# Optimization experiments

Measured on AMD Instinct MI355X. Metric: run time of the kernel, lower is better.

Reference implementation:

```python
import jax, jax.numpy as jnp
import numpy as np

EPS = 1e-5
NH, KD, D = 16, 16, 64  # num_heads, key_dim, per-head value dim (attn_ratio*key_dim)


def _bn(x, g, b):
    # train-mode BatchNorm1d over [B, C, N]: stats over (B, N), biased variance
    m = jnp.mean(x, axis=(0, 2), keepdims=True)
    v = jnp.var(x, axis=(0, 2), keepdims=True)
    return (x - m) * jax.lax.rsqrt(v + EPS) * g[None, :, None] + b[None, :, None]


def _relu6(x):
    return jnp.clip(x, 0.0, 6.0)


def setup_inputs() -> dict:
    key = jax.random.key(0)
    ks = jax.random.split(key, 8)
    B, C, H, W = 8, 256, 32, 32
    dim, dh, hid = 256, NH * D, 1024

    def w(k, shape):
        return jax.random.normal(k, shape, dtype=jnp.float32) * 0.02

    return {
        "x": jax.random.normal(ks[0], (B, C, H, W), dtype=jnp.float32),
        "g1": jnp.ones((dim,), jnp.float32), "b1": jnp.zeros((dim,), jnp.float32),
        "wq": w(ks[1], (NH * KD, dim)), "bq": jnp.zeros((NH * KD,), jnp.float32),
        "wk": w(ks[2], (NH * KD, dim)), "bk": jnp.zeros((NH * KD,), jnp.float32),
        "wv": w(ks[3], (dh, dim)), "bv": jnp.zeros((dh,), jnp.float32),
        "wp": w(ks[4], (dim, dh)), "bp": jnp.zeros((dim,), jnp.float32),
        "g2": jnp.ones((dim,), jnp.float32), "b2": jnp.zeros((dim,), jnp.float32),
        "w1": w(ks[5], (hid, dim)), "bb1": jnp.zeros((hid,), jnp.float32),
        "w2": w(ks[6], (dim, hid)), "bb2": jnp.zeros((dim,), jnp.float32),
    }


def reference(x, g1, b1, wq, bq, wk, bk, wv, bv, wp, bp, g2, b2, w1, bb1, w2, bb2):
    B, C, H, W = x.shape
    N = H * W
    xf = x.reshape(B, C, N)

    # --- attention branch (dropout is identity in eval/reference) ---
    y = _bn(xf, g1, b1)
    q = (jnp.einsum('bcn,oc->bon', y, wq) + bq[None, :, None]).reshape(B, NH, KD, N).transpose(0, 1, 3, 2)  # [B,h,N,kd]
    k = jnp.einsum('bcn,oc->bon', y, wk) + bk[None, :, None]
    k = k.reshape(B, NH, KD, N)                                                                           # [B,h,kd,N]
    v = (jnp.einsum('bcn,oc->bon', y, wv) + bv[None, :, None]).reshape(B, NH, D, N).transpose(0, 1, 3, 2)  # [B,h,N,d]
    # torch code divides by scale = key_dim**-0.5, i.e. multiplies by sqrt(key_dim)
    attn = jax.nn.softmax(jnp.einsum('bhnk,bhkm->bhnm', q, k) / (KD ** -0.5), axis=-1)
    o = jnp.einsum('bhnm,bhmd->bhnd', attn, v).transpose(0, 1, 3, 2).reshape(B, NH * D, N)                 # [B,dh,N]
    o = jnp.einsum('bdn,od->bon', o, wp) + bp[None, :, None]                                               # [B,C,N]
    xf = xf + o

    # --- MLP branch: Linear(dim->hid) + ReLU6 + Conv1d(hid->dim, k=1) ---
    y2 = _bn(xf, g2, b2)
    h = _relu6(jnp.einsum('bcn,hc->bhn', y2, w1) + bb1[None, :, None])
    m = jnp.einsum('bhn,oh->bon', h, w2) + bb2[None, :, None]
    xf = xf + m

    return xf.reshape(B, C, H, W)
```

## Files before the change

kernel.cpp:

```cpp
#include <hip/hip_runtime.h>
#include <hip/hip_bf16.h>
#include <cstdint>


typedef __attribute__((ext_vector_type(8))) short short8;
typedef __attribute__((ext_vector_type(4))) float floatx4;

#define QK_SC 5.770780163555851f

__device__ __forceinline__ float b2f(unsigned short u) {
  union { unsigned int i; float f; } x; x.i = ((unsigned int)u) << 16; return x.f;
}
__device__ __forceinline__ unsigned short f2b(float f) {
  union { float f; unsigned int i; } x; x.f = f;
  unsigned int r = x.i + 0x7FFFu + ((x.i >> 16) & 1u);
  return (unsigned short)(r >> 16);
}
__device__ __forceinline__ unsigned int f2b2(float a, float b) {
  __hip_bfloat162 h = __float22bfloat162_rn(make_float2(a, b));
  union { __hip_bfloat162 v; unsigned int u; } x; x.v = h; return x.u;
}
__device__ __forceinline__ void gload16(const unsigned short* g, unsigned short* l) {
  __builtin_amdgcn_global_load_lds(
      (const __attribute__((address_space(1))) unsigned int*)g,
      (__attribute__((address_space(3))) unsigned int*)l, 16, 0, 0);
}

__global__ __launch_bounds__(256) void prep(
    const float* __restrict__ s0, const float* __restrict__ s1,
    const float* __restrict__ s2, const float* __restrict__ s3,
    const float* __restrict__ s4, const float* __restrict__ s5,
    unsigned short* __restrict__ dst,
    const float* __restrict__ x, float* __restrict__ acc,
    const float* __restrict__ bq, const float* __restrict__ bk,
    const float* __restrict__ bv, float* __restrict__ biasqkv) {
  int blk = blockIdx.x, t = threadIdx.x;
  if (blk < 1152) {
    int i = blk * 256 + t;
    if (i >= 294912) return;
    const float* s; int li; size_t dbase;
    if (i < 16384)       { s = s0; li = i;          dbase = 0; }
    else if (i < 32768)  { s = s1; li = i - 16384;  dbase = 65536; }
    else if (i < 98304)  { s = s2; li = i - 32768;  dbase = 131072; }
    else if (i < 163840) { s = s3; li = i - 98304;  dbase = 393216; }
    else if (i < 229376) { s = s4; li = i - 163840; dbase = 655360; }
    else                 { s = s5; li = i - 229376; dbase = 917504; }
    float4 v = ((const float4*)s)[li];
    uint2 o; o.x = f2b2(v.x, v.y); o.y = f2b2(v.z, v.w);
    ((uint2*)(dst + dbase))[li] = o;
  } else if (blk < 3200) {
    int blk2 = blk - 1152;
    int b = blk2 >> 8, c = blk2 & 255;
    const float* p = x + (((size_t)(b * 256 + c)) << 10);
    float4 v = ((const float4*)p)[t];
    float s = (v.x + v.y) + (v.z + v.w);
    float s2 = (v.x * v.x + v.y * v.y) + (v.z * v.z + v.w * v.w);
    #pragma unroll
    for (int o = 32; o > 0; o >>= 1) { s += __shfl_down(s, o, 64); s2 += __shfl_down(s2, o, 64); }
    __shared__ float rs[4], rs2[4];
    int w = t >> 6;
    if ((t & 63) == 0) { rs[w] = s; rs2[w] = s2; }
    __syncthreads();
    if (t == 0) {
      atomicAdd(acc + c, (rs[0] + rs[1]) + (rs[2] + rs[3]));
      atomicAdd(acc + 256 + c, (rs2[0] + rs2[1]) + (rs2[2] + rs2[3]));
    }
  } else {
    int i = (blk - 3200) * 256 + t;
    float v = (i < 256) ? bq[i] : (i < 512) ? bk[i - 256] : bv[i - 512];
    biasqkv[i] = v;
  }
}

__global__ __launch_bounds__(256) void bn_apply_t(
    const float* __restrict__ x, const float* __restrict__ acc,
    const float* __restrict__ g, const float* __restrict__ bb,
    unsigned short* __restrict__ yt) {
  int nt = blockIdx.x, ct = blockIdx.y, b = blockIdx.z;
  int t = threadIdx.x;
  __shared__ unsigned short T[64][72];
  {
    int r = t >> 2, g4 = (t & 3) * 16;
    int c = ct * 64 + r;
    float m = acc[c] * (1.0f / 8192.0f);
    float var = acc[256 + c] * (1.0f / 8192.0f) - m * m;
    float scl = g[c] * rsqrtf(var + 1e-5f);
    float shf = bb[c] - m * scl;
    const float* p = x + (((size_t)(b * 256 + c)) << 10) + nt * 64 + g4;
    float4 u0 = *(const float4*)(p);
    float4 u1 = *(const float4*)(p + 4);
    float4 u2 = *(const float4*)(p + 8);
    float4 u3 = *(const float4*)(p + 12);
    uint4 o0, o1;
    o0.x = f2b2(fmaf(u0.x, scl, shf), fmaf(u0.y, scl, shf));
    o0.y = f2b2(fmaf(u0.z, scl, shf), fmaf(u0.w, scl, shf));
    o0.z = f2b2(fmaf(u1.x, scl, shf), fmaf(u1.y, scl, shf));
    o0.w = f2b2(fmaf(u1.z, scl, shf), fmaf(u1.w, scl, shf));
    o1.x = f2b2(fmaf(u2.x, scl, shf), fmaf(u2.y, scl, shf));
    o1.y = f2b2(fmaf(u2.z, scl, shf), fmaf(u2.w, scl, shf));
    o1.z = f2b2(fmaf(u3.x, scl, shf), fmaf(u3.y, scl, shf));
    o1.w = f2b2(fmaf(u3.z, scl, shf), fmaf(u3.w, scl, shf));
    *(uint4*)&T[r][g4] = o0;
    *(uint4*)&T[r][g4 + 8] = o1;
  }
  __syncthreads();
  {
    int nr = t >> 2, cg = (t & 3) * 16;
    unsigned int ob[8];
    #pragma unroll
    for (int j = 0; j < 8; ++j) {
      unsigned int lo = T[cg + 2 * j][nr];
      unsigned int hi = T[cg + 2 * j + 1][nr];
      ob[j] = lo | (hi << 16);
    }
    unsigned short* orow = yt + ((size_t)(b * 1024 + nt * 64 + nr)) * 256 + ct * 64 + cg;
    *(uint4*)&orow[0] = make_uint4(ob[0], ob[1], ob[2], ob[3]);
    *(uint4*)&orow[8] = make_uint4(ob[4], ob[5], ob[6], ob[7]);
  }
}

template <int MODE>
__global__ __launch_bounds__(256, 4) void gemm3(
    const unsigned short* __restrict__ W, const unsigned short* __restrict__ Bn,
    const float* __restrict__ bias, const float* __restrict__ resf,
    const unsigned short* __restrict__ resb, void* __restrict__ outv,
    float* __restrict__ stats, const float* __restrict__ bnin,
    const float* __restrict__ g, const float* __restrict__ bb, int M, int K) {
  int bid = blockIdx.x;
  int b = bid & 7;
  int rest = bid >> 3;
  int n0 = (rest & 15) * 64, m0 = (rest >> 4) * 64;
  int t = threadIdx.x, lane = t & 63, w = t >> 6;
  int ml = lane & 15, quad = lane >> 4;

  __shared__ unsigned short Wt[64][64];
  __shared__ unsigned short Yt[64][64];
  __shared__ float Scl[256], Shf[256];

  if (MODE == 6) {
    float m = bnin[t] * (1.0f / 8192.0f);
    float var = bnin[256 + t] * (1.0f / 8192.0f) - m * m;
    float scl = g[t] * rsqrtf(var + 1e-5f);
    Scl[t] = scl;
    Shf[t] = bb[t] - m * scl;
    __syncthreads();
  }

  const unsigned short* Bp = Bn + (size_t)b * 1024 * K;
  int sr = t >> 2, scg = (t & 3) * 16;
  const unsigned short* brow = Bp + (size_t)(n0 + sr) * K + scg;

  int lrow = lane >> 3;
  int cgs  = (lane & 7) ^ lrow;

  char* Wb = (char*)&Wt[0][0];
  char* Yb = (char*)&Yt[0][0];
  const int swa = (ml & 7) << 4;

  floatx4 acc[4];
  #pragma unroll
  for (int i = 0; i < 4; ++i) acc[i] = (floatx4){0.f, 0.f, 0.f, 0.f};

  for (int k0 = 0; k0 < K; k0 += 64) {
    #pragma unroll
    for (int j = 0; j < 2; ++j) {
      int row = w * 16 + j * 8 + lrow;
      gload16(W + (size_t)(m0 + row) * K + k0 + cgs * 8, &Wt[w * 16 + j * 8][0]);
    }
    if (MODE == 6) {
      uint4 r0 = *(const uint4*)(brow + k0);
      uint4 r1 = *(const uint4*)(brow + k0 + 8);
      int cb = k0 + scg;
      float4 s0 = *(const float4*)&Scl[cb],     h0 = *(const float4*)&Shf[cb];
      float4 s1 = *(const float4*)&Scl[cb + 4], h1 = *(const float4*)&Shf[cb + 4];
      float4 s2 = *(const float4*)&Scl[cb + 8], h2 = *(const float4*)&Shf[cb + 8];
      float4 s3 = *(const float4*)&Scl[cb + 12], h3 = *(const float4*)&Shf[cb + 12];
      uint4 o0, o1;
      o0.x = f2b2(fmaf(b2f(r0.x & 0xffff), s0.x, h0.x), fmaf(b2f(r0.x >> 16), s0.y, h0.y));
      o0.y = f2b2(fmaf(b2f(r0.y & 0xffff), s0.z, h0.z), fmaf(b2f(r0.y >> 16), s0.w, h0.w));
      o0.z = f2b2(fmaf(b2f(r0.z & 0xffff), s1.x, h1.x), fmaf(b2f(r0.z >> 16), s1.y, h1.y));
      o0.w = f2b2(fmaf(b2f(r0.w & 0xffff), s1.z, h1.z), fmaf(b2f(r0.w >> 16), s1.w, h1.w));
      o1.x = f2b2(fmaf(b2f(r1.x & 0xffff), s2.x, h2.x), fmaf(b2f(r1.x >> 16), s2.y, h2.y));
      o1.y = f2b2(fmaf(b2f(r1.y & 0xffff), s2.z, h2.z), fmaf(b2f(r1.y >> 16), s2.w, h2.w));
      o1.z = f2b2(fmaf(b2f(r1.z & 0xffff), s3.x, h3.x), fmaf(b2f(r1.z >> 16), s3.y, h3.y));
      o1.w = f2b2(fmaf(b2f(r1.w & 0xffff), s3.z, h3.z), fmaf(b2f(r1.w >> 16), s3.w, h3.w));
      int sg0 = (t & 3) * 2, sg1 = sg0 + 1;
      *(uint4*)(Yb + sr * 128 + ((sg0 ^ (sr & 7)) << 4)) = o0;
      *(uint4*)(Yb + sr * 128 + ((sg1 ^ (sr & 7)) << 4)) = o1;
    } else {
      #pragma unroll
      for (int j = 0; j < 2; ++j) {
        int row = w * 16 + j * 8 + lrow;
        gload16(Bp + (size_t)(n0 + row) * K + k0 + cgs * 8, &Yt[w * 16 + j * 8][0]);
      }
    }
    __syncthreads();
    int arow = w * 16 + ml;
    short8 a0 = *(const short8*)(Wb + arow * 128 + ((quad << 4) ^ swa));
    short8 a1 = *(const short8*)(Wb + arow * 128 + (((quad + 4) << 4) ^ swa));
    #pragma unroll
    for (int nt2 = 0; nt2 < 4; ++nt2) {
      int brw = nt2 * 16 + ml;
      short8 b0 = *(const short8*)(Yb + brw * 128 + ((quad << 4) ^ swa));
      short8 b1 = *(const short8*)(Yb + brw * 128 + (((quad + 4) << 4) ^ swa));
      acc[nt2] = __builtin_amdgcn_mfma_f32_16x16x32_bf16(a0, b0, acc[nt2], 0, 0, 0);
      acc[nt2] = __builtin_amdgcn_mfma_f32_16x16x32_bf16(a1, b1, acc[nt2], 0, 0, 0);
    }
    __syncthreads();
  }

  int row_base = m0 + w * 16 + quad * 4;

  if (MODE == 4) {
    int hh = row_base >> 4;
    float b0 = bias[row_base + 0], b1 = bias[row_base + 1];
    float b2 = bias[row_base + 2], b3 = bias[row_base + 3];
    if (hh < 32) {
      unsigned short* qkout = (unsigned short*)outv + ((hh < 16) ? 0 : 2097152);
      float os = (hh < 16) ? QK_SC : 1.0f;
      int head = hh & 15, kd0 = row_base & 15;
      #pragma unroll
      for (int c = 0; c < 4; ++c) {
        int col = n0 + c * 16 + ml;
        uint2 pw;
        pw.x = f2b2((acc[c][0] + b0) * os, (acc[c][1] + b1) * os);
        pw.y = f2b2((acc[c][2] + b2) * os, (acc[c][3] + b3) * os);
        *(uint2*)&qkout[(((size_t)b * 16 + head) * 1024 + col) * 16 + kd0] = pw;
      }
    } else {
      unsigned short* vout = (unsigned short*)outv + 4194304;
      int d0 = row_base - 512;
      #pragma unroll
      for (int c = 0; c < 4; ++c) {
        int col = n0 + c * 16 + ml;
        vout[((size_t)b * 1024 + d0 + 0) * 1024 + col] = f2b(acc[c][0] + b0);
        vout[((size_t)b * 1024 + d0 + 1) * 1024 + col] = f2b(acc[c][1] + b1);
        vout[((size_t)b * 1024 + d0 + 2) * 1024 + col] = f2b(acc[c][2] + b2);
        vout[((size_t)b * 1024 + d0 + 3) * 1024 + col] = f2b(acc[c][3] + b3);
      }
    }
  } else if (MODE == 5) {
    unsigned short* outp = (unsigned short*)outv;
    float vsum[4] = {0.f, 0.f, 0.f, 0.f}, vsq[4] = {0.f, 0.f, 0.f, 0.f};
    #pragma unroll
    for (int c = 0; c < 4; ++c) {
      int col = n0 + c * 16 + ml;
      float v0 = acc[c][0] + bias[row_base + 0] + resf[((size_t)b * 256 + row_base + 0) * 1024 + col];
      float v1 = acc[c][1] + bias[row_base + 1] + resf[((size_t)b * 256 + row_base + 1) * 1024 + col];
      float v2 = acc[c][2] + bias[row_base + 2] + resf[((size_t)b * 256 + row_base + 2) * 1024 + col];
      float v3 = acc[c][3] + bias[row_base + 3] + resf[((size_t)b * 256 + row_base + 3) * 1024 + col];
      vsum[0] += v0; vsq[0] += v0 * v0;
      vsum[1] += v1; vsq[1] += v1 * v1;
      vsum[2] += v2; vsq[2] += v2 * v2;
      vsum[3] += v3; vsq[3] += v3 * v3;
      uint2 pw; pw.x = f2b2(v0, v1); pw.y = f2b2(v2, v3);
      *(uint2*)&outp[((size_t)b * 1024 + col) * 256 + row_base] = pw;
    }
    #pragma unroll
    for (int r = 0; r < 4; ++r) {
      float s = vsum[r], q = vsq[r];
      #pragma unroll
      for (int o = 1; o < 16; o <<= 1) { s += __shfl_xor(s, o, 64); q += __shfl_xor(q, o, 64); }
      if (ml == 0) {
        atomicAdd(stats + row_base + r, s);
        atomicAdd(stats + 256 + row_base + r, q);
      }
    }
  } else if (MODE == 6) {
    unsigned short* outp = (unsigned short*)outv;
    #pragma unroll
    for (int c = 0; c < 4; ++c) {
      int col = n0 + c * 16 + ml;
      float v0 = fminf(fmaxf(acc[c][0] + bias[row_base + 0], 0.f), 6.f);
      float v1 = fminf(fmaxf(acc[c][1] + bias[row_base + 1], 0.f), 6.f);
      float v2 = fminf(fmaxf(acc[c][2] + bias[row_base + 2], 0.f), 6.f);
      float v3 = fminf(fmaxf(acc[c][3] + bias[row_base + 3], 0.f), 6.f);
      uint2 pw; pw.x = f2b2(v0, v1); pw.y = f2b2(v2, v3);
      *(uint2*)&outp[((size_t)b * 1024 + col) * 1024 + row_base] = pw;
    }
  } else {
    float* outp = (float*)outv;
    #pragma unroll
    for (int c = 0; c < 4; ++c) {
      int col = n0 + c * 16 + ml;
      uint2 rv = *(const uint2*)(resb + ((size_t)b * 1024 + col) * 256 + row_base);
      float r0 = b2f((unsigned short)(rv.x & 0xffff));
      float r1 = b2f((unsigned short)(rv.x >> 16));
      float r2 = b2f((unsigned short)(rv.y & 0xffff));
      float r3 = b2f((unsigned short)(rv.y >> 16));
      outp[((size_t)b * 256 + row_base + 0) * 1024 + col] = acc[c][0] + bias[row_base + 0] + r0;
      outp[((size_t)b * 256 + row_base + 1) * 1024 + col] = acc[c][1] + bias[row_base + 1] + r1;
      outp[((size_t)b * 256 + row_base + 2) * 1024 + col] = acc[c][2] + bias[row_base + 2] + r2;
      outp[((size_t)b * 256 + row_base + 3) * 1024 + col] = acc[c][3] + bias[row_base + 3] + r3;
    }
  }
}

__global__ __launch_bounds__(256, 4) void attn_kernel(
    const unsigned short* __restrict__ qt, const unsigned short* __restrict__ kt,
    const unsigned short* __restrict__ vt, unsigned short* __restrict__ ot) {
  int bx0 = blockIdx.x;
  int bx = (bx0 & 7) * 128 + (bx0 >> 3);
  int nt = bx & 7, h = (bx >> 3) & 15, b = bx >> 7;
  int tid = threadIdx.x, lane = tid & 63, w = tid >> 6;
  int ml = lane & 15, quad = lane >> 4;

  __shared__ unsigned int Pscr[4][2][2][16][18];
  __shared__ float Ssum[4][2][16];

  const int n0 = nt * 128 + w * 32;
  const size_t qk_row = ((size_t)b * 16 + h) * 1024;

  short8 qf[2];
  #pragma unroll
  for (int rg = 0; rg < 2; ++rg) {
    short8 z = {0, 0, 0, 0, 0, 0, 0, 0};
    if (quad < 2)
      z = *(const short8*)(qt + (qk_row + n0 + rg * 16 + ml) * 16 + quad * 8);
    qf[rg] = z;
  }

  const floatx4 zf = {0.f, 0.f, 0.f, 0.f};
  floatx4 oacc[2][4];
  #pragma unroll
  for (int rg = 0; rg < 2; ++rg)
    #pragma unroll
    for (int dt = 0; dt < 4; ++dt) oacc[rg][dt] = zf;
  float psum0 = 0.f, psum1 = 0.f;

  const unsigned short* kp = kt + qk_row * 16;
  const unsigned short* vp = vt + ((size_t)b * 1024 + h * 64) * 1024;

  #pragma unroll 2
  for (int mc = 0; mc < 1024; mc += 32) {
    int buf = (mc >> 5) & 1;
    short8 kf[2];
    #pragma unroll
    for (int tt = 0; tt < 2; ++tt) {
      short8 z = {0, 0, 0, 0, 0, 0, 0, 0};
      if (quad < 2)
        z = *(const short8*)(kp + (size_t)(mc + tt * 16 + ml) * 16 + quad * 8);
      kf[tt] = z;
    }
    short8 vf[4];
    #pragma unroll
    for (int dt = 0; dt < 4; ++dt)
      vf[dt] = *(const short8*)(vp + (size_t)(dt * 16 + ml) * 1024 + mc + quad * 8);

    #pragma unroll
    for (int rg = 0; rg < 2; ++rg) {
      #pragma unroll
      for (int tt = 0; tt < 2; ++tt) {
        floatx4 s = __builtin_amdgcn_mfma_f32_16x16x32_bf16(kf[tt], qf[rg], zf, 0, 0, 0);
        float p0 = __builtin_amdgcn_exp2f(s[0]);
        float p1 = __builtin_amdgcn_exp2f(s[1]);
        float p2 = __builtin_amdgcn_exp2f(s[2]);
        float p3 = __builtin_amdgcn_exp2f(s[3]);
        if (rg == 0) psum0 += (p0 + p1) + (p2 + p3);
        else         psum1 += (p0 + p1) + (p2 + p3);
        uint2 pw; pw.x = f2b2(p0, p1); pw.y = f2b2(p2, p3);
        *(uint2*)&Pscr[w][buf][rg][ml][tt * 8 + quad * 2] = pw;
      }
    }
    #pragma unroll
    for (int rg = 0; rg < 2; ++rg) {
      uint2 a0 = *(const uint2*)&Pscr[w][buf][rg][ml][quad * 4];
      uint2 a1 = *(const uint2*)&Pscr[w][buf][rg][ml][quad * 4 + 2];
      union { uint4 u; short8 s; } cv;
      cv.u = make_uint4(a0.x, a0.y, a1.x, a1.y);
      short8 af = cv.s;
      #pragma unroll
      for (int dt = 0; dt < 4; ++dt)
        oacc[rg][dt] = __builtin_amdgcn_mfma_f32_16x16x32_bf16(af, vf[dt], oacc[rg][dt], 0, 0, 0);
    }
  }

  {
    float s0 = psum0;
    s0 += __shfl_xor(s0, 16, 64);
    s0 += __shfl_xor(s0, 32, 64);
    float s1 = psum1;
    s1 += __shfl_xor(s1, 16, 64);
    s1 += __shfl_xor(s1, 32, 64);
    if (lane < 16) { Ssum[w][0][ml] = s0; Ssum[w][1][ml] = s1; }
  }
  #pragma unroll
  for (int rg = 0; rg < 2; ++rg) {
    float4 sv = *(const float4*)&Ssum[w][rg][quad * 4];
    float inv0 = 1.0f / sv.x, inv1 = 1.0f / sv.y;
    float inv2 = 1.0f / sv.z, inv3 = 1.0f / sv.w;
    int nbase = n0 + rg * 16 + quad * 4;
    #pragma unroll
    for (int dt = 0; dt < 4; ++dt) {
      int dg = h * 64 + dt * 16 + ml;
      size_t obase = (((size_t)b << 10) + nbase) * 1024 + dg;
      ot[obase + 0 * 1024] = f2b(oacc[rg][dt][0] * inv0);
      ot[obase + 1 * 1024] = f2b(oacc[rg][dt][1] * inv1);
      ot[obase + 2 * 1024] = f2b(oacc[rg][dt][2] * inv2);
      ot[obase + 3 * 1024] = f2b(oacc[rg][dt][3] * inv3);
    }
  }
}

extern "C" void kernel_launch(void* const* d_in, const int* in_sizes, int n_in,
                              void* d_out, int out_size, void* d_ws, size_t ws_size,
                              hipStream_t stream) {
  const float* x   = (const float*)d_in[0];
  const float* g1  = (const float*)d_in[1];
  const float* b1  = (const float*)d_in[2];
  const float* wq  = (const float*)d_in[3];
  const float* bq  = (const float*)d_in[4];
  const float* wk  = (const float*)d_in[5];
  const float* bk  = (const float*)d_in[6];
  const float* wv  = (const float*)d_in[7];
  const float* bv  = (const float*)d_in[8];
  const float* wp  = (const float*)d_in[9];
  const float* bp  = (const float*)d_in[10];
  const float* g2  = (const float*)d_in[11];
  const float* b2  = (const float*)d_in[12];
  const float* w1  = (const float*)d_in[13];
  const float* bb1 = (const float*)d_in[14];
  const float* w2  = (const float*)d_in[15];
  const float* bb2 = (const float*)d_in[16];

  char* ws = (char*)d_ws;
  float* bnacc   = (float*)ws;
  float* biasqkv = (float*)(ws + 4096);
  unsigned short* y_t  = (unsigned short*)(ws + 16384);
  unsigned short* qt   = y_t + (size_t)2 * 1024 * 1024;
  unsigned short* kt   = qt  + (size_t)2 * 1024 * 1024;
  unsigned short* vt   = kt  + (size_t)2 * 1024 * 1024;
  unsigned short* ot   = vt  + (size_t)8 * 1024 * 1024;
  unsigned short* xf1t = ot  + (size_t)8 * 1024 * 1024;
  unsigned short* wb   = xf1t + (size_t)2 * 1024 * 1024;
  unsigned short* hb_t = ot;
  float* outp = (float*)d_out;

  unsigned short* wqkvb = wb;
  unsigned short* wpb = wb + 393216;
  unsigned short* w1b = wb + 655360;
  unsigned short* w2b = wb + 917504;
  const unsigned short* nub = nullptr;
  const float* nuf = nullptr;

  hipMemsetAsync(bnacc, 0, 4096, stream);
  prep<<<dim3(3206), dim3(256), 0, stream>>>(
      wq, wk, wv, wp, w1, w2, wb, x, bnacc, bq, bk, bv, biasqkv);

  bn_apply_t<<<dim3(16, 4, 8), dim3(256), 0, stream>>>(x, bnacc, g1, b1, y_t);
  gemm3<4><<<dim3(3072), dim3(256), 0, stream>>>(
      wqkvb, y_t, biasqkv, nuf, nub, qt, nullptr, nuf, nuf, nuf, 1536, 256);
  attn_kernel<<<dim3(1024), dim3(256), 0, stream>>>(qt, kt, vt, ot);
  gemm3<5><<<dim3(512), dim3(256), 0, stream>>>(
      wpb, ot, bp, x, nub, xf1t, bnacc + 512, nuf, nuf, nuf, 256, 1024);

  gemm3<6><<<dim3(2048), dim3(256), 0, stream>>>(
      w1b, xf1t, bb1, nuf, nub, hb_t, nullptr, bnacc + 512, g2, b2, 1024, 256);
  gemm3<7><<<dim3(512), dim3(256), 0, stream>>>(
      w2b, hb_t, bb2, nuf, xf1t, outp, nullptr, nuf, nuf, nuf, 256, 1024);
}
```

Before: 239.9 us.

## Software-pipeline attention loop with register double-buffered K/V loads

```diff
diff --git a/kernel.cpp b/kernel.cpp
--- a/kernel.cpp
+++ b/kernel.cpp
@@ -296,7 +296,58 @@
   }
 }
 
-__global__ __launch_bounds__(256, 4) void attn_kernel(
+#define LOADK(dst, mc)                                                         \
+  {                                                                            \
+    _Pragma("unroll") for (int tt = 0; tt < 2; ++tt) {                         \
+      short8 z = {0, 0, 0, 0, 0, 0, 0, 0};                                     \
+      if (quad < 2)                                                            \
+        z = *(const short8*)(kp + (size_t)((mc) + tt * 16 + ml) * 16 + quad * 8); \
+      dst[tt] = z;                                                             \
+    }                                                                          \
+  }
+
+#define LOADV(dst, mc)                                                         \
+  {                                                                            \
+    _Pragma("unroll") for (int dt = 0; dt < 4; ++dt)                           \
+      dst[dt] = *(const short8*)(vp + (size_t)(dt * 16 + ml) * 1024 + (mc) + quad * 8); \
+  }
+
+#define QKSTEP(kf, bufidx)                                                     \
+  {                                                                            \
+    _Pragma("unroll") for (int rg = 0; rg < 2; ++rg) {                         \
+      _Pragma("unroll") for (int tt = 0; tt < 2; ++tt) {                       \
+        floatx4 s = __builtin_amdgcn_mfma_f32_16x16x32_bf16(kf[tt], qf[rg], zf, 0, 0, 0); \
+        float p0 = __builtin_amdgcn_exp2f(s[0]);                               \
+        float p1 = __builtin_amdgcn_exp2f(s[1]);                               \
+        float p2 = __builtin_amdgcn_exp2f(s[2]);                               \
+        float p3 = __builtin_amdgcn_exp2f(s[3]);                               \
+        if (rg == 0) psum0 += (p0 + p1) + (p2 + p3);                           \
+        else         psum1 += (p0 + p1) + (p2 + p3);                           \
+        uint2 pw; pw.x = f2b2(p0, p1); pw.y = f2b2(p2, p3);                    \
+        *(uint2*)&Pscr[w][bufidx][rg][ml][tt * 8 + quad * 2] = pw;             \
+      }                                                                        \
+    }                                                                          \
+  }
+
+#define READP(bufidx, pa)                                                      \
+  {                                                                            \
+    _Pragma("unroll") for (int rg = 0; rg < 2; ++rg) {                         \
+      uint2 a0 = *(const uint2*)&Pscr[w][bufidx][rg][ml][quad * 4];            \
+      uint2 a1 = *(const uint2*)&Pscr[w][bufidx][rg][ml][quad * 4 + 2];        \
+      union { uint4 u; short8 s; } cv;                                         \
+      cv.u = make_uint4(a0.x, a0.y, a1.x, a1.y);                               \
+      pa[rg] = cv.s;                                                           \
+    }                                                                          \
+  }
+
+#define PVSTEP(pa, vf)                                                         \
+  {                                                                            \
+    _Pragma("unroll") for (int rg = 0; rg < 2; ++rg)                           \
+      _Pragma("unroll") for (int dt = 0; dt < 4; ++dt)                         \
+        oacc[rg][dt] = __builtin_amdgcn_mfma_f32_16x16x32_bf16(pa[rg], vf[dt], oacc[rg][dt], 0, 0, 0); \
+  }
+
+__global__ __launch_bounds__(256, 2) void attn_kernel(
     const unsigned short* __restrict__ qt, const unsigned short* __restrict__ kt,
     const unsigned short* __restrict__ vt, unsigned short* __restrict__ ot) {
   int bx0 = blockIdx.x;
@@ -331,49 +382,31 @@
   const unsigned short* kp = kt + qk_row * 16;
   const unsigned short* vp = vt + ((size_t)b * 1024 + h * 64) * 1024;
 
-  #pragma unroll 2
-  for (int mc = 0; mc < 1024; mc += 32) {
-    int buf = (mc >> 5) & 1;
-    short8 kf[2];
-    #pragma unroll
-    for (int tt = 0; tt < 2; ++tt) {
-      short8 z = {0, 0, 0, 0, 0, 0, 0, 0};
-      if (quad < 2)
-        z = *(const short8*)(kp + (size_t)(mc + tt * 16 + ml) * 16 + quad * 8);
-      kf[tt] = z;
-    }
-    short8 vf[4];
-    #pragma unroll
-    for (int dt = 0; dt < 4; ++dt)
-      vf[dt] = *(const short8*)(vp + (size_t)(dt * 16 + ml) * 1024 + mc + quad * 8);
-
-    #pragma unroll
-    for (int rg = 0; rg < 2; ++rg) {
-      #pragma unroll
-      for (int tt = 0; tt < 2; ++tt) {
-        floatx4 s = __builtin_amdgcn_mfma_f32_16x16x32_bf16(kf[tt], qf[rg], zf, 0, 0, 0);
-        float p0 = __builtin_amdgcn_exp2f(s[0]);
-        float p1 = __builtin_amdgcn_exp2f(s[1]);
-        float p2 = __builtin_amdgcn_exp2f(s[2]);
-        float p3 = __builtin_amdgcn_exp2f(s[3]);
-        if (rg == 0) psum0 += (p0 + p1) + (p2 + p3);
-        else         psum1 += (p0 + p1) + (p2 + p3);
-        uint2 pw; pw.x = f2b2(p0, p1); pw.y = f2b2(p2, p3);
-        *(uint2*)&Pscr[w][buf][rg][ml][tt * 8 + quad * 2] = pw;
-      }
-    }
-    #pragma unroll
-    for (int rg = 0; rg < 2; ++rg) {
-      uint2 a0 = *(const uint2*)&Pscr[w][buf][rg][ml][quad * 4];
-      uint2 a1 = *(const uint2*)&Pscr[w][buf][rg][ml][quad * 4 + 2];
-      union { uint4 u; short8 s; } cv;
-      cv.u = make_uint4(a0.x, a0.y, a1.x, a1.y);
-      short8 af = cv.s;
-      #pragma unroll
-      for (int dt = 0; dt < 4; ++dt)
-        oacc[rg][dt] = __builtin_amdgcn_mfma_f32_16x16x32_bf16(af, vf[dt], oacc[rg][dt], 0, 0, 0);
-    }
-  }
+  short8 kfA[2], kfB[2], vfA[4], vfB[4], pa[2];
+
+  LOADK(kfA, 0); LOADV(vfA, 0);
+  QKSTEP(kfA, 0);
+  LOADK(kfB, 32); LOADV(vfB, 32);
+
+  for (int j = 0; j < 15; ++j) {
+    int mc = j * 64;
+    READP(0, pa);
+    QKSTEP(kfB, 1);
+    LOADK(kfA, mc + 64);
+    PVSTEP(pa, vfA);
+    LOADV(vfA, mc + 64);
+    READP(1, pa);
+    QKSTEP(kfA, 0);
+    LOADK(kfB, mc + 96);
+    PVSTEP(pa, vfB);
+    LOADV(vfB, mc + 96);
+  }
+
+  READP(0, pa);
+  QKSTEP(kfB, 1);
+  PVSTEP(pa, vfA);
+  READP(1, pa);
+  PVSTEP(pa, vfB);
 
   {
     float s0 = psum0;
```

After: 256.1 us. 6.8% more time.

## Stage K/V tiles through double-buffered LDS with async global loads in attention

Applied to the files above, without the earlier changes.

```diff
diff --git a/kernel.cpp b/kernel.cpp
--- a/kernel.cpp
+++ b/kernel.cpp
@@ -307,6 +307,8 @@
 
   __shared__ unsigned int Pscr[4][2][2][16][18];
   __shared__ float Ssum[4][2][16];
+  __shared__ unsigned short Kt[2][32][16];
+  __shared__ unsigned short Vt[2][64][32];
 
   const int n0 = nt * 128 + w * 32;
   const size_t qk_row = ((size_t)b * 16 + h) * 1024;
@@ -331,21 +333,34 @@
   const unsigned short* kp = kt + qk_row * 16;
   const unsigned short* vp = vt + ((size_t)b * 1024 + h * 64) * 1024;
 
-  #pragma unroll 2
-  for (int mc = 0; mc < 1024; mc += 32) {
-    int buf = (mc >> 5) & 1;
+  int vrow = w * 16 + (lane >> 2);
+  int vcg  = (lane & 3) ^ ((lane >> 2) & 3);
+
+  auto stageKV = [&](int buf, int mc) {
+    gload16(vp + (size_t)vrow * 1024 + mc + vcg * 8, &Vt[buf][w * 16][0]);
+    if (w == 0)
+      gload16(kp + (size_t)mc * 16 + lane * 8, &Kt[buf][0][0]);
+  };
+
+  stageKV(0, 0);
+  __syncthreads();
+
+  for (int it = 0; it < 32; ++it) {
+    int buf = it & 1;
+    int mc = it << 5;
+    if (it < 31) stageKV(buf ^ 1, mc + 32);
+
+    const char* Kb = (const char*)&Kt[buf][0][0];
+    const char* Vb = (const char*)&Vt[buf][0][0];
+    const short8 z8 = {0, 0, 0, 0, 0, 0, 0, 0};
     short8 kf[2];
     #pragma unroll
-    for (int tt = 0; tt < 2; ++tt) {
-      short8 z = {0, 0, 0, 0, 0, 0, 0, 0};
-      if (quad < 2)
-        z = *(const short8*)(kp + (size_t)(mc + tt * 16 + ml) * 16 + quad * 8);
-      kf[tt] = z;
-    }
+    for (int tt = 0; tt < 2; ++tt)
+      kf[tt] = (quad < 2) ? *(const short8*)(Kb + (tt * 16 + ml) * 32 + quad * 16) : z8;
     short8 vf[4];
     #pragma unroll
     for (int dt = 0; dt < 4; ++dt)
-      vf[dt] = *(const short8*)(vp + (size_t)(dt * 16 + ml) * 1024 + mc + quad * 8);
+      vf[dt] = *(const short8*)(Vb + (dt * 16 + ml) * 64 + ((quad ^ (ml & 3)) << 4));
 
     #pragma unroll
     for (int rg = 0; rg < 2; ++rg) {
@@ -373,6 +388,7 @@
       for (int dt = 0; dt < 4; ++dt)
         oacc[rg][dt] = __builtin_amdgcn_mfma_f32_16x16x32_bf16(af, vf[dt], oacc[rg][dt], 0, 0, 0);
     }
+    __syncthreads();
   }
 
   {
```

Result: faster. 208.7 us (-13.0%).
